# Performance work log

Measured on AMD Instinct MI355X. Metric: run time of the kernel, lower is better.

## Reference

```python
import jax, jax.numpy as jnp
import numpy as np

B, C, H, W = 8, 256, 80, 160   # 1/8-resolution feature maps of a 640x1280 stereo pair
DISP = 192 // 8                 # cost volume depth at 1/8 res
FACTOR = 2 ** 3                 # convex-upsample factor (n_downsample=3)
TOP_K = 3


def setup_inputs() -> dict:
    key = jax.random.key(0)
    k1, k2, k3 = jax.random.split(key, 3)
    return {
        "left": jax.random.normal(k1, (B, C, H, W), dtype=jnp.float32),
        "right": jax.random.normal(k2, (B, C, H, W), dtype=jnp.float32),
        "mask": jax.random.normal(k3, (B, 9 * FACTOR * FACTOR, H, W), dtype=jnp.float32),
        "iters": 12,
    }


def build_cost_volume(left, right):
    # cost[b,i,h,w] = mean_c left[b,c,h,w] * right[b,c,h,w-i], zero where w < i
    slices = []
    for i in range(DISP):  # fixed small structural loop over disparity shifts
        prod = jnp.mean(left[:, :, :, i:] * right[:, :, :, : W - i if i > 0 else W], axis=1)
        prod = jnp.pad(prod, ((0, 0), (0, 0), (i, 0)))
        slices.append(prod)
    return jnp.stack(slices, axis=1)  # [B, DISP, H, W]


def regression_topk(cost, k=TOP_K):
    # top-k over the disparity axis, softmax-weighted expectation of indices
    c = jnp.moveaxis(cost, 1, -1)            # [B, H, W, DISP]
    vals, inds = jax.lax.top_k(c, k)          # descending, like torch sort(1, True)[:, :k]
    w = jax.nn.softmax(vals, axis=-1)
    disp = jnp.sum(w * inds.astype(vals.dtype), axis=-1)
    return disp[:, None]                      # [B, 1, H, W]


def convex_upsample(flow, mask, iters):
    # Upsample [H,W] flow -> [8H,8W] via softmax convex combination of 3x3 neighbors.
    N, D, Hh, Ww = flow.shape
    temp = 1.0 + jnp.exp(-(jnp.float32(iters) - 1.0))  # training-mode temperature
    m = mask.reshape(N, 1, 9, FACTOR, FACTOR, Hh, Ww)
    m = jax.nn.softmax(m / temp, axis=2)
    fp = jnp.pad(FACTOR * flow, ((0, 0), (0, 0), (1, 1), (1, 1)))
    # 3x3 unfold in torch F.unfold row-major order: (dy, dx)
    patches = jnp.stack(
        [fp[:, :, dy:dy + Hh, dx:dx + Ww] for dy in range(3) for dx in range(3)], axis=2
    )  # [N, D, 9, H, W]
    up = jnp.sum(m * patches[:, :, :, None, None], axis=2)   # [N, D, F, F, H, W]
    up = up.transpose(0, 1, 4, 2, 5, 3)                      # [N, D, H, F, W, F]
    return up.reshape(N, D, FACTOR * Hh, FACTOR * Ww)


def reference(left, right, mask, iters):
    cost = build_cost_volume(left, right)
    init_disp = regression_topk(cost)                               # [B,1,H,W]
    # flow field (x-disparity channel + frozen y channel, as delta_flow[:,1]=0)
    flow = jnp.concatenate([init_disp, jnp.zeros_like(init_disp)], axis=1)
    flow_up = convex_upsample(flow, mask, iters)                    # [B,2,8H,8W]
    return -flow_up[:, :1]                                          # disparity prediction
```

## Files before the change

### kernel.cpp

```cpp
#include <hip/hip_runtime.h>
#include <cmath>

#define NBATCH 8
#define NCH    256
#define NH     80
#define NW     160
#define NDISP  24
#define FAC    8

constexpr int TPB1  = 256;
constexpr int WPB   = 4;
constexpr int NTILE = 5;
constexpr int SLOTS = 192;
constexpr int NBUF  = 4;

typedef __attribute__((address_space(1))) unsigned int gu32;
typedef __attribute__((address_space(3))) unsigned int lu32;

#define LDS_AUX 2

__device__ __forceinline__ void gload_lds16(const float* g, float4* l) {
  __builtin_amdgcn_global_load_lds((gu32*)g, (lu32*)l, 16, 0, LDS_AUX);
}

template <int N>
__device__ __forceinline__ void wait_vm() {
  if constexpr (N == 9)      asm volatile("s_waitcnt vmcnt(9)" ::: "memory");
  else if constexpr (N == 6) asm volatile("s_waitcnt vmcnt(6)" ::: "memory");
  else if constexpr (N == 3) asm volatile("s_waitcnt vmcnt(3)" ::: "memory");
  else                       asm volatile("s_waitcnt vmcnt(0)" ::: "memory");
  __builtin_amdgcn_sched_barrier(0);
}

__device__ __forceinline__ void wait_lgkm0() {
  asm volatile("s_waitcnt lgkmcnt(0)" ::: "memory");
  __builtin_amdgcn_sched_barrier(0);
}

__device__ __forceinline__ float f4c(const float4& v, int k) {
  switch (k) { case 0: return v.x; case 1: return v.y; case 2: return v.z; default: return v.w; }
}

__global__ __launch_bounds__(TPB1) void cost_topk_kernel(
    const float* __restrict__ left, const float* __restrict__ right,
    float* __restrict__ disp)
{
  __shared__ float4 lds4[WPB][NBUF][SLOTS];

  const int lane = threadIdx.x & 63;
  const int widx = threadIdx.x >> 6;
  const int wid  = blockIdx.x * WPB + widx;
  const int tile = wid % NTILE;
  const int row  = wid / NTILE;
  const int b    = row / NH;
  const int h    = row % NH;
  const int wb   = tile * 32;

  const int cg = lane & 7;
  const int wq = lane >> 3;

  const size_t hw = (size_t)NH * NW;
  const float* lrow = left  + (size_t)b * NCH * hw + (size_t)h * NW;
  const float* rrow = right + (size_t)b * NCH * hw + (size_t)h * NW;

  const int c0 = lane >> 4,        q0 = (lane & 15) ^ c0;
  const int c1 = 4 + (lane >> 4),  q1 = (lane & 15) ^ c1;
  const int cl = lane >> 3,        wqs = (lane & 7) ^ cl;

  int off0 = wb - 32 + 4 * q0; if (off0 < 0) off0 = 0;
  int off1 = wb - 32 + 4 * q1; if (off1 < 0) off1 = 0;

  const float* srcR0 = rrow + (size_t)(c0 * 32) * hw + off0;
  const float* srcR1 = rrow + (size_t)(c1 * 32) * hw + off1;
  const float* srcL  = lrow + (size_t)(cl * 32) * hw + wb + 4 * wqs;

  float4* const wbase = &lds4[widx][0][0];

#define STAGE(BP) do {                               \
    gload_lds16(srcR0, (BP));                        \
    gload_lds16(srcR1, (BP) + 64);                   \
    gload_lds16(srcL,  (BP) + 128);                  \
    srcR0 += hw; srcR1 += hw; srcL += hw; } while (0)

  int rsl[7];
#pragma unroll
  for (int k = 0; k < 7; ++k) rsl[k] = cg * 16 + ((wq + 2 + k) ^ cg);
  const int lslot = 128 + cg * 8 + (wq ^ cg);

  float acc[NDISP][4];
#pragma unroll
  for (int i = 0; i < NDISP; ++i)
#pragma unroll
    for (int ws = 0; ws < 4; ++ws) acc[i][ws] = 0.f;

  auto fmastep = [&](const float4* base) {
    float4 Lq = base[lslot];
    float4 Qa = base[rsl[0]];
#pragma unroll
    for (int g = 0; g < 6; ++g) {
      float4 Qb = base[rsl[g + 1]];
      const int i0 = 20 - 4 * g;
#pragma unroll
      for (int di = 0; di < 4; ++di)
#pragma unroll
        for (int ws = 0; ws < 4; ++ws) {
          const int pos = ws - di + 4;
          float rv = (pos < 4) ? f4c(Qa, pos) : f4c(Qb, pos - 4);
          acc[i0 + di][ws] = __builtin_fmaf(f4c(Lq, ws), rv, acc[i0 + di][ws]);
        }
      Qa = Qb;
    }
  };

  const float4 fzero{0.f, 0.f, 0.f, 0.f};
  const int azslot = (lane >> 3) * 16 + (lane & 7);

  STAGE(wbase + 0 * SLOTS);
  STAGE(wbase + 1 * SLOTS);
  STAGE(wbase + 2 * SLOTS);

#pragma unroll 4
  for (int j = 0; j < 28; ++j) {
    float4* bs = wbase + ((j + 3) & 3) * SLOTS;
    float4* bc = wbase + (j & 3) * SLOTS;
    wait_lgkm0();
    STAGE(bs);
    wait_vm<9>();
    if (tile == 0) bc[azslot] = fzero;
    fmastep(bc);
  }
  {
    float4* bs = wbase + 3 * SLOTS;
    float4* bc = wbase + 0 * SLOTS;
    wait_lgkm0(); STAGE(bs); wait_vm<9>();
    if (tile == 0) bc[azslot] = fzero;
    fmastep(bc);
  }
  { float4* bc = wbase + 1 * SLOTS; wait_vm<6>(); if (tile == 0) bc[azslot] = fzero; fmastep(bc); }
  { float4* bc = wbase + 2 * SLOTS; wait_vm<3>(); if (tile == 0) bc[azslot] = fzero; fmastep(bc); }
  { float4* bc = wbase + 3 * SLOTS; wait_vm<0>(); if (tile == 0) bc[azslot] = fzero; fmastep(bc); }
#undef STAGE

#pragma unroll
  for (int mskm = 1; mskm < 8; mskm <<= 1)
#pragma unroll
    for (int i = 0; i < NDISP; ++i)
#pragma unroll
      for (int ws = 0; ws < 4; ++ws)
        acc[i][ws] += __shfl_xor(acc[i][ws], mskm, 64);

  if (cg == 0) {
    float o[4];
#pragma unroll
    for (int ws = 0; ws < 4; ++ws) {
      float v1 = -1e30f, v2 = -1e30f, v3 = -1e30f;
      int   j1 = 0, j2 = 0, j3 = 0;
#pragma unroll
      for (int i = 0; i < NDISP; ++i) {
        float v = acc[i][ws] * 0.00390625f;
        if (v > v1)      { v3 = v2; j3 = j2; v2 = v1; j2 = j1; v1 = v; j1 = i; }
        else if (v > v2) { v3 = v2; j3 = j2; v2 = v;  j2 = i; }
        else if (v > v3) { v3 = v;  j3 = i; }
      }
      float e2 = expf(v2 - v1), e3 = expf(v3 - v1);
      float ssum = 1.0f + e2 + e3;
      o[ws] = ((float)j1 + e2 * (float)j2 + e3 * (float)j3) / ssum;
    }
    *reinterpret_cast<float4*>(&disp[((size_t)b * NH + h) * NW + wb + wq * 4]) =
        float4{o[0], o[1], o[2], o[3]};
  }
}

__global__ __launch_bounds__(256) void upsample_kernel(
    const float* __restrict__ disp, const float* __restrict__ mask,
    const int* __restrict__ itp, float* __restrict__ out)
{
  int idx = blockIdx.x * 256 + threadIdx.x;
  const int w  = idx % NW;
  const int fy = (idx / NW) & 7;
  const int h  = (idx / (NW * FAC)) % NH;
  const int b  = idx / (NW * FAC * NH);

  const float iters = (float)itp[0];
  const float temp  = 1.0f + __expf(-(iters - 1.0f));
  const float sc    = 1.44269504088896340736f / temp;

  const size_t hw = (size_t)NH * NW;
  const float* drow = disp + (size_t)b * hw;
  float d[9];
#pragma unroll
  for (int dy = 0; dy < 3; ++dy)
#pragma unroll
    for (int dx = 0; dx < 3; ++dx) {
      int h2 = h + dy - 1, w2 = w + dx - 1;
      bool ok = (h2 >= 0) && (h2 < NH) && (w2 >= 0) && (w2 < NW);
      d[dy * 3 + dx] = ok ? drow[h2 * NW + w2] : 0.f;
    }

  const float* mb = mask + (size_t)b * 576 * hw + (size_t)h * NW + w;
  float m[9][FAC];
#pragma unroll
  for (int j = 0; j < 9; ++j)
#pragma unroll
    for (int fx = 0; fx < FAC; ++fx)
      m[j][fx] = mb[(size_t)((j * 8 + fy) * 8 + fx) * hw];

  float o[FAC];
#pragma unroll
  for (int fx = 0; fx < FAC; ++fx) {
    float mx = m[0][fx];
#pragma unroll
    for (int j = 1; j < 9; ++j) mx = fmaxf(mx, m[j][fx]);
    float ssum = 0.f, accv = 0.f;
#pragma unroll
    for (int j = 0; j < 9; ++j) {
      float e = exp2f((m[j][fx] - mx) * sc);
      ssum += e;
      accv += e * d[j];
    }
    o[fx] = (-8.0f * accv) * __builtin_amdgcn_rcpf(ssum);
  }

  float* op = out + ((size_t)b * (NH * FAC) + (size_t)(h * FAC + fy)) * (NW * FAC) + (size_t)w * FAC;
  *reinterpret_cast<float4*>(op)     = float4{o[0], o[1], o[2], o[3]};
  *reinterpret_cast<float4*>(op + 4) = float4{o[4], o[5], o[6], o[7]};
}

extern "C" void kernel_launch(void* const* d_in, const int* in_sizes, int n_in,
                              void* d_out, int out_size, void* d_ws, size_t ws_size,
                              hipStream_t stream) {
  (void)in_sizes; (void)n_in; (void)out_size; (void)ws_size;
  const float* left  = (const float*)d_in[0];
  const float* right = (const float*)d_in[1];
  const float* mask  = (const float*)d_in[2];
  const int*   iters = (const int*)d_in[3];
  float* out  = (float*)d_out;
  float* disp = (float*)d_ws;

  hipLaunchKernelGGL(cost_topk_kernel, dim3(NBATCH * NH * NTILE / WPB), dim3(TPB1), 0, stream,
                     left, right, disp);
  hipLaunchKernelGGL(upsample_kernel, dim3(NBATCH * NH * FAC * NW / 256), dim3(256), 0, stream,
                     disp, mask, iters, out);
}
```

Measured before the change: 126.7 us.

## Split channel reduction across two waves per tile with LDS reduction

Each output tile is now handled by a block of two waves. Each wave processes half the channels (16 stages instead of 32) using a double-buffered LDS pipeline instead of a quad-buffered one. The partial cost sums are combined through LDS before top-k. This doubles the number of waves to hide latency and shortens each wave's serial loop. In exchange it adds a block barrier, an LDS reduction, and a shallower prefetch depth.

```diff
diff --git a/kernel.cpp b/kernel.cpp
--- a/kernel.cpp
+++ b/kernel.cpp
@@ -8,11 +8,12 @@
 #define NDISP  24
 #define FAC    8
 
-constexpr int TPB1  = 256;
-constexpr int WPB   = 4;
+constexpr int TPB1  = 128;
+constexpr int WPB   = 2;
 constexpr int NTILE = 5;
 constexpr int SLOTS = 192;
-constexpr int NBUF  = 4;
+constexpr int NBUF  = 2;
+constexpr int NSTEP = 16;
 
 typedef __attribute__((address_space(1))) unsigned int gu32;
 typedef __attribute__((address_space(3))) unsigned int lu32;
@@ -25,9 +26,7 @@
 
 template <int N>
 __device__ __forceinline__ void wait_vm() {
-  if constexpr (N == 9)      asm volatile("s_waitcnt vmcnt(9)" ::: "memory");
-  else if constexpr (N == 6) asm volatile("s_waitcnt vmcnt(6)" ::: "memory");
-  else if constexpr (N == 3) asm volatile("s_waitcnt vmcnt(3)" ::: "memory");
+  if constexpr (N == 3)      asm volatile("s_waitcnt vmcnt(3)" ::: "memory");
   else                       asm volatile("s_waitcnt vmcnt(0)" ::: "memory");
   __builtin_amdgcn_sched_barrier(0);
 }
@@ -49,12 +48,13 @@
 
   const int lane = threadIdx.x & 63;
   const int widx = threadIdx.x >> 6;
-  const int wid  = blockIdx.x * WPB + widx;
-  const int tile = wid % NTILE;
-  const int row  = wid / NTILE;
+  const int tileid = blockIdx.x;
+  const int tile = tileid % NTILE;
+  const int row  = tileid / NTILE;
   const int b    = row / NH;
   const int h    = row % NH;
   const int wb   = tile * 32;
+  const int chb  = widx * NSTEP;
 
   const int cg = lane & 7;
   const int wq = lane >> 3;
@@ -70,9 +70,9 @@
   int off0 = wb - 32 + 4 * q0; if (off0 < 0) off0 = 0;
   int off1 = wb - 32 + 4 * q1; if (off1 < 0) off1 = 0;
 
-  const float* srcR0 = rrow + (size_t)(c0 * 32) * hw + off0;
-  const float* srcR1 = rrow + (size_t)(c1 * 32) * hw + off1;
-  const float* srcL  = lrow + (size_t)(cl * 32) * hw + wb + 4 * wqs;
+  const float* srcR0 = rrow + (size_t)(c0 * 32 + chb) * hw + off0;
+  const float* srcR1 = rrow + (size_t)(c1 * 32 + chb) * hw + off1;
+  const float* srcL  = lrow + (size_t)(cl * 32 + chb) * hw + wb + 4 * wqs;
 
   float4* const wbase = &lds4[widx][0][0];
 
@@ -116,29 +116,20 @@
   const int azslot = (lane >> 3) * 16 + (lane & 7);
 
   STAGE(wbase + 0 * SLOTS);
-  STAGE(wbase + 1 * SLOTS);
-  STAGE(wbase + 2 * SLOTS);
-
-#pragma unroll 4
-  for (int j = 0; j < 28; ++j) {
-    float4* bs = wbase + ((j + 3) & 3) * SLOTS;
-    float4* bc = wbase + (j & 3) * SLOTS;
+
+#pragma unroll 2
+  for (int j = 0; j < NSTEP; ++j) {
     wait_lgkm0();
-    STAGE(bs);
-    wait_vm<9>();
+    if (j + 1 < NSTEP) {
+      STAGE(wbase + ((j + 1) & 1) * SLOTS);
+      wait_vm<3>();
+    } else {
+      wait_vm<0>();
+    }
+    float4* bc = wbase + (j & 1) * SLOTS;
     if (tile == 0) bc[azslot] = fzero;
     fmastep(bc);
   }
-  {
-    float4* bs = wbase + 3 * SLOTS;
-    float4* bc = wbase + 0 * SLOTS;
-    wait_lgkm0(); STAGE(bs); wait_vm<9>();
-    if (tile == 0) bc[azslot] = fzero;
-    fmastep(bc);
-  }
-  { float4* bc = wbase + 1 * SLOTS; wait_vm<6>(); if (tile == 0) bc[azslot] = fzero; fmastep(bc); }
-  { float4* bc = wbase + 2 * SLOTS; wait_vm<3>(); if (tile == 0) bc[azslot] = fzero; fmastep(bc); }
-  { float4* bc = wbase + 3 * SLOTS; wait_vm<0>(); if (tile == 0) bc[azslot] = fzero; fmastep(bc); }
 #undef STAGE
 
 #pragma unroll
@@ -149,8 +140,22 @@
       for (int ws = 0; ws < 4; ++ws)
         acc[i][ws] += __shfl_xor(acc[i][ws], mskm, 64);
 
-  if (cg == 0) {
+  if (widx == 1 && cg == 0) {
+    float4* red = &lds4[1][0][0];
+#pragma unroll
+    for (int i = 0; i < NDISP; ++i)
+      red[wq * NDISP + i] = float4{acc[i][0], acc[i][1], acc[i][2], acc[i][3]};
+  }
+  __syncthreads();
+
+  if (widx == 0 && cg == 0) {
+    const float4* red = &lds4[1][0][0];
     float o[4];
+#pragma unroll
+    for (int i = 0; i < NDISP; ++i) {
+      float4 r = red[wq * NDISP + i];
+      acc[i][0] += r.x; acc[i][1] += r.y; acc[i][2] += r.z; acc[i][3] += r.w;
+    }
 #pragma unroll
     for (int ws = 0; ws < 4; ++ws) {
       float v1 = -1e30f, v2 = -1e30f, v3 = -1e30f;
@@ -237,7 +242,7 @@
   float* out  = (float*)d_out;
   float* disp = (float*)d_ws;
 
-  hipLaunchKernelGGL(cost_topk_kernel, dim3(NBATCH * NH * NTILE / WPB), dim3(TPB1), 0, stream,
+  hipLaunchKernelGGL(cost_topk_kernel, dim3(NBATCH * NH * NTILE), dim3(TPB1), 0, stream,
                      left, right, disp);
   hipLaunchKernelGGL(upsample_kernel, dim3(NBATCH * NH * FAC * NW / 256), dim3(256), 0, stream,
                      disp, mask, iters, out);
```

New measurement: 130.2 us (median of 2 runs). 1.03x slower.
